# Performance work log

Hardware: AMD Instinct MI355X
Metric: run time of the kernel (lower is better)

The kernel has to match this reference:

```python
import jax, jax.numpy as jnp
import numpy as np

NMS_MAX_OUTPUTS = 2000
CLS_SCORE_THRESH = 0.7
IOU_THRESH = 0.3
USE_SIDE_REFINE = False
B, N_ANCHORS, N_VALID, NUM_CLASSES = 4, 20000, 12000, 2


def setup_inputs() -> dict:
    key = jax.random.key(0)
    k = jax.random.split(key, 7)
    deltas = 0.5 * jax.random.normal(k[0], (B, N_ANCHORS, 2), jnp.float32)
    side_deltas = 0.5 * jax.random.normal(k[1], (B, N_ANCHORS, 1), jnp.float32)
    class_logits = 2.0 * jax.random.normal(k[2], (B, N_ANCHORS, NUM_CLASSES), jnp.float32)
    # CTPN-style anchors: fixed width 16, heights in [11, 280], on a ~1600px page
    cx = jax.random.uniform(k[3], (N_VALID,), jnp.float32, 8.0, 1592.0)
    cy = jax.random.uniform(k[4], (N_VALID,), jnp.float32, 0.0, 1600.0)
    h = jax.random.uniform(k[5], (N_VALID,), jnp.float32, 11.0, 280.0)
    valid_anchors = jnp.stack([cx - 8.0, cy - h * 0.5, cx + 8.0, cy + h * 0.5], axis=1)
    valid_indices = jnp.sort(
        jax.random.choice(k[6], N_ANCHORS, (N_VALID,), replace=False)
    ).astype(jnp.int32)
    return {
        "deltas": deltas,
        "side_deltas": side_deltas,
        "class_logits": class_logits,
        "valid_anchors": valid_anchors,
        "valid_indices": valid_indices,
    }


def apply_regress(deltas, side_deltas, anchors, use_side_refine):
    # deltas [B,V,2], side_deltas [B,V,1], anchors [V,4] -> [B,V,4]
    w = anchors[:, 2] - anchors[:, 0]
    h = anchors[:, 3] - anchors[:, 1]
    cx = (anchors[:, 0] + anchors[:, 2]) * 0.5
    cy = (anchors[:, 1] + anchors[:, 3]) * 0.5
    d = jnp.concatenate([deltas, side_deltas], axis=-1) * jnp.array([0.1, 0.2, 0.1], deltas.dtype)
    dy, dh, dx = d[..., 0], d[..., 1], d[..., 2]
    cy = cy + dy * h
    cx = cx + dx * w
    h = h * jnp.exp(dh)
    y1 = cy - h * 0.5
    y2 = cy + h * 0.5
    if use_side_refine:
        x1 = jnp.maximum(cx - w * 0.5, 0.0)
        x2 = cx + w * 0.5
    else:
        x1 = jnp.broadcast_to(anchors[:, 0], y1.shape)
        x2 = jnp.broadcast_to(anchors[:, 2], y1.shape)
    return jnp.stack([x1, y1, x2, y2], axis=-1)


def nms_single(boxes, scores, logits, max_out, iou_t, score_t):
    """Greedy NMS (tf.image.non_max_suppression semantics) + gather + pad_to_fixed_size."""
    V = boxes.shape[0]
    order = jnp.argsort(-jax.lax.stop_gradient(scores))
    b, s, l = boxes[order], scores[order], logits[order]
    bc = jax.lax.stop_gradient(b)  # suppression decisions are non-differentiable
    x1, y1, x2, y2 = bc[:, 0], bc[:, 1], bc[:, 2], bc[:, 3]
    areas = (x2 - x1) * (y2 - y1)
    idxs = jnp.arange(V)
    valid = jax.lax.stop_gradient(s) > score_t

    def body(i, keep):
        xx1 = jnp.maximum(x1[i], x1)
        yy1 = jnp.maximum(y1[i], y1)
        xx2 = jnp.minimum(x2[i], x2)
        yy2 = jnp.minimum(y2[i], y2)
        inter = jnp.maximum(xx2 - xx1, 0.0) * jnp.maximum(yy2 - yy1, 0.0)
        iou = inter / (areas[i] + areas - inter + 1e-10)
        sup = (iou > iou_t) & (idxs > i)
        return jnp.where(keep[i], keep & ~sup, keep)

    keep = jax.lax.fori_loop(0, V, body, valid)
    rank = jnp.cumsum(keep.astype(jnp.int32)) - 1
    sel = keep & (rank < max_out)
    dest = jnp.where(sel, rank, max_out)  # overflow rows parked at row max_out, sliced off
    tag = jnp.ones((V, 1), b.dtype)

    def pad_fixed(x):
        # append tag column of 1s for real rows, scatter to fixed size, zero-pad rest
        aug = jnp.where(sel[:, None], jnp.concatenate([x, tag], axis=1), 0.0)
        out = jnp.zeros((max_out + 1, aug.shape[1]), aug.dtype).at[dest].set(aug)
        return out[:max_out]

    return pad_fixed(b), pad_fixed(s[:, None]), pad_fixed(l)


def reference(deltas, side_deltas, class_logits, valid_anchors, valid_indices):
    d = jnp.take(deltas, valid_indices, axis=1)
    sd = jnp.take(side_deltas, valid_indices, axis=1)
    cl = jnp.take(class_logits, valid_indices, axis=1)
    class_scores = jax.nn.softmax(cl, axis=-1)
    fg_scores = jnp.max(class_scores[..., 1:], axis=-1)  # [B,V]
    proposals = apply_regress(d, sd, valid_anchors, USE_SIDE_REFINE)  # [B,V,4]
    f = lambda bb, ss, ll: nms_single(bb, ss, ll, NMS_MAX_OUTPUTS, IOU_THRESH, CLS_SCORE_THRESH)
    boxes, box_scores, out_logits = jax.vmap(f)(proposals, fg_scores, cl)
    return boxes, box_scores, out_logits
```

## Files before the change

kernel.cpp:

```cpp
#include <hip/hip_runtime.h>
#include <cstdint>
#include <cstddef>

typedef unsigned long long u64;
typedef unsigned int u32;
typedef u32 u32x4 __attribute__((ext_vector_type(4)));

#define AS1 __attribute__((address_space(1)))
#define AS3 __attribute__((address_space(3)))

constexpr int kB = 4;
constexpr int kNA = 20000;
constexpr int kV = 12000;
constexpr int kCAP = 5120;
constexpr int kW = kCAP / 64;
constexpr int kIC = 256;
constexpr int kMAXOUT = 2000;
constexpr int kGPB = 20;
constexpr float kIOU = 0.3f;
constexpr float kSCORE = 0.7f;

static __device__ __forceinline__ u64 greedy64(u64 freeS, u32 d_lo, u32 d_hi) {
  u64 keptS;
  asm volatile(
      "s_mov_b64 s[40:41], %[free]\n\t"
      "s_mov_b64 s[42:43], 0\n\t"
      "GRD_%=:\n\t"
      "s_ff1_i32_b64 s44, s[40:41]\n\t"
      "s_cmp_eq_i32 s44, -1\n\t"
      "s_cbranch_scc1 GRDEND_%=\n\t"
      "s_bitset1_b64 s[42:43], s44\n\t"
      "s_bitset0_b64 s[40:41], s44\n\t"
      "v_readlane_b32 s46, %[dlo], s44\n\t"
      "v_readlane_b32 s47, %[dhi], s44\n\t"
      "s_nop 4\n\t"
      "s_andn2_b64 s[40:41], s[40:41], s[46:47]\n\t"
      "s_branch GRD_%=\n\t"
      "GRDEND_%=:\n\t"
      "s_mov_b64 %[kept], s[42:43]\n\t"
      : [kept] "=&s"(keptS)
      : [free] "s"(freeS), [dlo] "v"(d_lo), [dhi] "v"(d_hi)
      : "s40", "s41", "s42", "s43", "s44", "s45", "s46", "s47", "scc");
  return keptS;
}

__device__ __forceinline__ u64 waveOr64(u64 v) {
  v |= __shfl_xor((unsigned long long)v, 32, 64);
  v |= __shfl_xor((unsigned long long)v, 16, 64);
  v |= __shfl_xor((unsigned long long)v, 8, 64);
  v |= __shfl_xor((unsigned long long)v, 4, 64);
  v |= __shfl_xor((unsigned long long)v, 2, 64);
  v |= __shfl_xor((unsigned long long)v, 1, 64);
  return v;
}

__device__ __forceinline__ u64 readlane64u(u64 v, int l) {
  u32 lo = __builtin_amdgcn_readlane((u32)v, (u32)l);
  u32 hi = __builtin_amdgcn_readlane((u32)(v >> 32), (u32)l);
  return ((u64)hi << 32) | lo;
}

__global__ __launch_bounds__(256) void stage_score(
    const float* __restrict__ deltas, const float* __restrict__ logits,
    const float* __restrict__ anchors, const int* __restrict__ vidx,
    u32* __restrict__ counts, u64* __restrict__ keys,
    float* __restrict__ rec_y1, float* __restrict__ rec_y2,
    float* __restrict__ rec_l0, float* __restrict__ rec_l1) {
  int t = blockIdx.x * 256 + threadIdx.x;
  if (t >= kB * kV) return;
  int b = t / kV, i = t - b * kV;
  int lane = threadIdx.x & 63;
  int idx = vidx[i];
  float2 lg = *(const float2*)(logits + ((size_t)b * kNA + idx) * 2);
  float score = 1.0f / (1.0f + expf(lg.x - lg.y));
  if (!(score > kSCORE)) return;
  float2 dd = *(const float2*)(deltas + ((size_t)b * kNA + idx) * 2);
  float4 a = *(const float4*)(anchors + (size_t)i * 4);
  float h = a.w - a.y;
  float cy = (a.y + a.w) * 0.5f + (dd.x * 0.1f) * h;
  float hn = h * expf(dd.y * 0.2f);
  rec_y1[t] = cy - hn * 0.5f;
  rec_y2[t] = cy + hn * 0.5f;
  rec_l0[t] = lg.x;
  rec_l1[t] = lg.y;
  u64 act = __ballot(1);
  int b0 = (int)__builtin_amdgcn_readfirstlane((u32)b);
  u64 sameb = __ballot(b == b0);
  u64 grp = (b == b0) ? sameb : (act & ~sameb);
  u32 cnt = (u32)__popcll(grp);
  int lead = (int)__ffsll((unsigned long long)grp) - 1;
  u32 base = 0;
  if (lane == lead) base = atomicAdd(&counts[b], cnt);
  base = (u32)__shfl((int)base, lead, 64);
  u32 pos = base + (u32)__popcll(grp & ((1ULL << lane) - 1ULL));
  if (pos < kCAP) {
    u64 key = ((u64)(0xFFFFFFFFu - __float_as_uint(score)) << 32) | (u32)i;
    keys[(size_t)b * kCAP + pos] = key;
  }
}

__global__ __launch_bounds__(256) void rank_sort_emit(
    const u32* __restrict__ counts, const u64* __restrict__ keys,
    const float* __restrict__ rec_y1, const float* __restrict__ rec_y2,
    const float* __restrict__ rec_l0, const float* __restrict__ rec_l1,
    const float* __restrict__ anchors,
    float4* __restrict__ sbox, float* __restrict__ sarea,
    float* __restrict__ ssc, float* __restrict__ sl0, float* __restrict__ sl1) {
  __shared__ u64 sk[kCAP];
  int b = blockIdx.x / (kCAP / 256);
  int chunk = blockIdx.x % (kCAP / 256);
  int tid = threadIdx.x;
  int cnt = (int)min(counts[b], (u32)kCAP);
  for (int e = tid; e < kCAP; e += 256)
    sk[e] = (e < cnt) ? keys[(size_t)b * kCAP + e] : ~0ULL;
  __syncthreads();
  int s = chunk * 256 + tid;
  if (s >= cnt) return;
  u64 ks = sk[s];
  int rank = 0;
  for (int j = 0; j < kCAP; j += 8) {
#pragma unroll
    for (int u = 0; u < 8; ++u) rank += (sk[j + u] < ks) ? 1 : 0;
  }
  int i = (int)(u32)ks;
  float sc = __uint_as_float(0xFFFFFFFFu - (u32)(ks >> 32));
  float x1 = anchors[(size_t)i * 4 + 0], x2 = anchors[(size_t)i * 4 + 2];
  float y1 = rec_y1[b * kV + i], y2 = rec_y2[b * kV + i];
  size_t o = (size_t)b * kCAP + rank;
  sbox[o] = make_float4(x1, y1, x2, y2);
  sarea[o] = (x2 - x1) * (y2 - y1);
  ssc[o] = sc;
  sl0[o] = rec_l0[b * kV + i];
  sl1[o] = rec_l1[b * kV + i];
}

__global__ __launch_bounds__(256) void stage_mask(
    const u32* __restrict__ counts,
    const float4* __restrict__ sbox, const float* __restrict__ sarea,
    u64* __restrict__ mask) {
  __shared__ float4 sb[4][kIC];
  __shared__ float sa[4][kIC];
  int lane = threadIdx.x & 63;
  int wv = threadIdx.x >> 6;
  int gw = blockIdx.x * 4 + wv;
  int bt = gw & 3;
  int rest = gw >> 2;
  int jb = rest % kW;
  int ic = rest / kW;
  int M = (int)min(counts[bt], (u32)kCAP);
  int W = (M + 63) >> 6;
  if (jb >= W) return;
  int ibeg = ic * kIC;
  int iend = min(min(M, jb * 64 + 64), ibeg + kIC);
  if (ibeg >= iend) return;
  const float4* pb = sbox + (size_t)bt * kCAP;
  const float* pa = sarea + (size_t)bt * kCAP;
  u64* mb = mask + (size_t)bt * ((size_t)kW * kCAP);
#pragma unroll
  for (int r = 0; r < kIC / 64; ++r) {
    int e = r * 64 + lane;
    sb[wv][e] = pb[ibeg + e];
    sa[wv][e] = pa[ibeg + e];
  }
  int j = jb * 64 + lane;
  bool jv = (j < M);
  float4 bj = make_float4(0.f, 0.f, 0.f, 0.f);
  float aj = 0.f;
  if (jv) { bj = pb[j]; aj = pa[j]; }
  for (int b0 = ibeg; b0 < iend; b0 += 64) {
    int lim = min(iend - b0, 64);
    u64 mywm = 0;
#pragma unroll 4
    for (int k = 0; k < lim; ++k) {
      int e = b0 - ibeg + k;
      float4 bi = sb[wv][e];
      float ai = sa[wv][e];
      float xx1 = fmaxf(bi.x, bj.x);
      float yy1 = fmaxf(bi.y, bj.y);
      float xx2 = fminf(bi.z, bj.z);
      float yy2 = fminf(bi.w, bj.w);
      float inter = fmaxf(xx2 - xx1, 0.0f) * fmaxf(yy2 - yy1, 0.0f);
      float iou = inter / (ai + aj - inter + 1e-10f);
      bool sup = jv && (j > b0 + k) && (iou > kIOU);
      u64 wm = __ballot(sup);
      if (k == lane) mywm = wm;
    }
    if (lane < lim)
      mb[(((size_t)(b0 >> 6)) * kW + jb) * 64 + lane] = mywm;
  }
}

__global__ __launch_bounds__(64, 1) void stage_scan(
    const u32* __restrict__ counts, const u64* __restrict__ mask,
    u64* __restrict__ pub,
    const float4* __restrict__ sbox, const float* __restrict__ ssc,
    const float* __restrict__ sl0, const float* __restrict__ sl1,
    float* __restrict__ out) {
  __shared__ __align__(16) u64 col[20224];
  const int bid = blockIdx.x;
  const int bt = bid & 3;
  const int g = bid >> 2;
  const int lane = threadIdx.x;
  const int M = (int)min(counts[bt], (u32)kCAP);
  const int W = (M + 63) >> 6;
  const int blk0 = 4 * g;
  if (blk0 >= W) return;
  const u64* mb = mask + (size_t)bt * ((size_t)kW * kCAP);
  u64* pp = pub + (size_t)(bt * kGPB) * 8;

  const int nu = min(4 * g + 4, 78);
  for (int b = 0; b < nu; ++b) {
    __builtin_amdgcn_global_load_lds(
        (const AS1 u32*)(mb + ((size_t)b * kW + blk0) * 64 + (size_t)lane * 2),
        (AS3 u32*)&col[b * 256], 16, 0, 0);
    __builtin_amdgcn_global_load_lds(
        (const AS1 u32*)(mb + ((size_t)b * kW + blk0 + 2) * 64 + (size_t)lane * 2),
        (AS3 u32*)&col[b * 256 + 128], 16, 0, 0);
  }
  if (g == 19) {
    __builtin_amdgcn_global_load_lds(
        (const AS1 u32*)(mb + ((size_t)78 * kW + 78) * 64 + (size_t)lane * 2),
        (AS3 u32*)&col[19968], 16, 0, 0);
    __builtin_amdgcn_global_load_lds(
        (const AS1 u32*)(mb + ((size_t)79 * kW + 78) * 64 + (size_t)lane * 2),
        (AS3 u32*)&col[20096], 16, 0, 0);
  }
  __builtin_amdgcn_s_waitcnt(0x0070);

  auto wpv = [&](int b, int wq) -> const u64* {
    if (b >= 78) return &col[19968 + (b - 78) * 128 + (wq - 2) * 64];
    return &col[b * 256 + wq * 64];
  };

  u64 acc0 = 0, acc1 = 0, acc2 = 0, acc3 = 0;
  u32 cum = 0;
  const u64* qa = pp + (size_t)lane * 2;
  const u64* qb = pp + 128 + (size_t)(lane & 15) * 2;
  int next = 0;
  while (next < g) {
    u32x4 ra, rb;
    asm volatile(
        "global_load_dwordx4 %0, %2, off sc0 sc1\n\t"
        "global_load_dwordx4 %1, %3, off sc0 sc1\n\t"
        "s_waitcnt vmcnt(0)"
        : "=&v"(ra), "=&v"(rb)
        : "v"(qa), "v"(qb)
        : "memory");
    u64 wA0 = ((u64)ra[1] << 32) | ra[0];
    u64 wA1 = ((u64)ra[3] << 32) | ra[2];
    u64 wB0 = ((u64)rb[1] << 32) | rb[0];
    u64 wB1 = ((u64)rb[3] << 32) | rb[2];
    u64 okA = __ballot(((wA0 & wA1) >> 63) != 0);
    u64 okB = __ballot(((wB0 & wB1) >> 63) != 0);
    int w = next;
    for (; w < g; ++w) {
      u64 km0, km1, km2, km3;
      if (w < 16) {
        if (((okA >> (4 * w)) & 0xFULL) != 0xFULL) break;
        int L = 4 * w;
        km0 = (u64)(u32)readlane64u(wA0, L)     | ((u64)(u32)readlane64u(wA1, L) << 32);
        km1 = (u64)(u32)readlane64u(wA0, L + 1) | ((u64)(u32)readlane64u(wA1, L + 1) << 32);
        km2 = (u64)(u32)readlane64u(wA0, L + 2) | ((u64)(u32)readlane64u(wA1, L + 2) << 32);
        km3 = (u64)(u32)readlane64u(wA0, L + 3) | ((u64)(u32)readlane64u(wA1, L + 3) << 32);
      } else {
        int L = 4 * (w - 16);
        if (((okB >> L) & 0xFULL) != 0xFULL) break;
        km0 = (u64)(u32)readlane64u(wB0, L)     | ((u64)(u32)readlane64u(wB1, L) << 32);
        km1 = (u64)(u32)readlane64u(wB0, L + 1) | ((u64)(u32)readlane64u(wB1, L + 1) << 32);
        km2 = (u64)(u32)readlane64u(wB0, L + 2) | ((u64)(u32)readlane64u(wB1, L + 2) << 32);
        km3 = (u64)(u32)readlane64u(wB0, L + 3) | ((u64)(u32)readlane64u(wB1, L + 3) << 32);
      }
      cum += (u32)__popcll(km0) + (u32)__popcll(km1) +
             (u32)__popcll(km2) + (u32)__popcll(km3);
      if (km0 | km1 | km2 | km3) {
        u64 m0 = -(u64)((km0 >> lane) & 1ULL);
        u64 m1 = -(u64)((km1 >> lane) & 1ULL);
        u64 m2 = -(u64)((km2 >> lane) & 1ULL);
        u64 m3 = -(u64)((km3 >> lane) & 1ULL);
        const u64* p0 = &col[(4 * w + 0) * 256];
        const u64* p1 = &col[(4 * w + 1) * 256];
        const u64* p2 = &col[(4 * w + 2) * 256];
        const u64* p3 = &col[(4 * w + 3) * 256];
        u64 v0 = (p0[lane] & m0) | (p1[lane] & m1) | (p2[lane] & m2) | (p3[lane] & m3);
        u64 v1 = (p0[64 + lane] & m0) | (p1[64 + lane] & m1) | (p2[64 + lane] & m2) | (p3[64 + lane] & m3);
        u64 v2 = (p0[128 + lane] & m0) | (p1[128 + lane] & m1) | (p2[128 + lane] & m2) | (p3[128 + lane] & m3);
        u64 v3 = (p0[192 + lane] & m0) | (p1[192 + lane] & m1) | (p2[192 + lane] & m2) | (p3[192 + lane] & m3);
        acc0 |= waveOr64(v0);
        acc1 |= waveOr64(v1);
        acc2 |= waveOr64(v2);
        acc3 |= waveOr64(v3);
      }
    }
    next = w;
    if (next < g) __builtin_amdgcn_s_sleep(8);
  }

  u64 km[4];
  u32 cums[4];
#define OWN_BLOCK(J, ACC)                                                     \
  {                                                                           \
    const int blk = blk0 + (J);                                               \
    cums[J] = cum;                                                            \
    u64 k = 0;                                                                \
    if (blk < W && (int)cum < kMAXOUT) {                                      \
      int remn = M - blk * 64;                                                \
      u64 validm = (remn >= 64) ? ~0ULL : ((1ULL << remn) - 1ULL);            \
      u64 freeb = ~(ACC)&validm;                                              \
      u32 flo = __builtin_amdgcn_readfirstlane((u32)freeb);                   \
      u32 fhi = __builtin_amdgcn_readfirstlane((u32)(freeb >> 32));           \
      u64 diag = wpv(blk, J)[lane];                                           \
      k = greedy64(((u64)fhi << 32) | flo, (u32)diag, (u32)(diag >> 32));     \
    }                                                                         \
    km[J] = k;                                                                \
    cum += (u32)__popcll(k);                                                  \
  }
  OWN_BLOCK(0, acc0)
  if (km[0]) {
    u64 m = -(u64)((km[0] >> lane) & 1ULL);
    acc1 |= waveOr64(wpv(blk0, 1)[lane] & m);
    acc2 |= waveOr64(wpv(blk0, 2)[lane] & m);
    acc3 |= waveOr64(wpv(blk0, 3)[lane] & m);
  }
  OWN_BLOCK(1, acc1)
  if (km[1]) {
    u64 m = -(u64)((km[1] >> lane) & 1ULL);
    acc2 |= waveOr64(wpv(blk0 + 1, 2)[lane] & m);
    acc3 |= waveOr64(wpv(blk0 + 1, 3)[lane] & m);
  }
  OWN_BLOCK(2, acc2)
  if (km[2]) {
    u64 m = -(u64)((km[2] >> lane) & 1ULL);
    acc3 |= waveOr64(wpv(blk0 + 2, 3)[lane] & m);
  }
  OWN_BLOCK(3, acc3)
#undef OWN_BLOCK

  if (lane == 0) {
    const u64 F = 1ULL << 63;
#pragma unroll
    for (int c = 0; c < 4; ++c) {
      (void)__hip_atomic_fetch_or(&pp[(size_t)g * 8 + 2 * c], F | (u64)(u32)km[c],
                                  __ATOMIC_RELAXED, __HIP_MEMORY_SCOPE_AGENT);
      (void)__hip_atomic_fetch_or(&pp[(size_t)g * 8 + 2 * c + 1], F | (u64)(u32)(km[c] >> 32),
                                  __ATOMIC_RELAXED, __HIP_MEMORY_SCOPE_AGENT);
    }
  }

  float* boxes = out;
  float* bscores = out + (size_t)kB * kMAXOUT * 5;
  float* blogits = out + (size_t)kB * kMAXOUT * 7;
  auto emit = [&](int i, int rank) {
    size_t o = (size_t)bt * kCAP + i;
    float4 bx = sbox[o];
    size_t t = (size_t)bt * kMAXOUT + rank;
    boxes[t * 5 + 0] = bx.x;
    boxes[t * 5 + 1] = bx.y;
    boxes[t * 5 + 2] = bx.z;
    boxes[t * 5 + 3] = bx.w;
    boxes[t * 5 + 4] = 1.0f;
    bscores[t * 2 + 0] = ssc[o];
    bscores[t * 2 + 1] = 1.0f;
    blogits[t * 3 + 0] = sl0[o];
    blogits[t * 3 + 1] = sl1[o];
    blogits[t * 3 + 2] = 1.0f;
  };
#pragma unroll
  for (int c = 0; c < 4; ++c) {
    if ((km[c] >> lane) & 1ULL) {
      int rank = (int)cums[c] + (int)__popcll(km[c] & ((1ULL << lane) - 1ULL));
      if (rank < kMAXOUT) emit((blk0 + c) * 64 + lane, rank);
    }
  }
}

extern "C" void kernel_launch(void* const* d_in, const int* in_sizes, int n_in,
                              void* d_out, int out_size, void* d_ws, size_t ws_size,
                              hipStream_t stream) {
  const float* deltas = (const float*)d_in[0];
  const float* logits = (const float*)d_in[2];
  const float* anchors = (const float*)d_in[3];
  const int* vidx = (const int*)d_in[4];
  float* out = (float*)d_out;

  char* p = (char*)d_ws;
  auto take = [&](size_t bytes) -> char* {
    char* r = p;
    p += (bytes + 255) & ~(size_t)255;
    return r;
  };
  u32* counts = (u32*)take(kB * sizeof(u32));
  u64* pub = (u64*)take((size_t)kB * kGPB * 8 * sizeof(u64));
  u64* keys = (u64*)take((size_t)kB * kCAP * sizeof(u64));
  float* rec_y1 = (float*)take((size_t)kB * kV * sizeof(float));
  float* rec_y2 = (float*)take((size_t)kB * kV * sizeof(float));
  float* rec_l0 = (float*)take((size_t)kB * kV * sizeof(float));
  float* rec_l1 = (float*)take((size_t)kB * kV * sizeof(float));
  float4* sbox = (float4*)take((size_t)kB * kCAP * sizeof(float4));
  float* sarea = (float*)take((size_t)kB * kCAP * sizeof(float));
  float* ssc = (float*)take((size_t)kB * kCAP * sizeof(float));
  float* sl0 = (float*)take((size_t)kB * kCAP * sizeof(float));
  float* sl1 = (float*)take((size_t)kB * kCAP * sizeof(float));
  u64* mask = (u64*)take((size_t)kB * kCAP * kW * sizeof(u64) + 4096);

  (void)hipMemsetAsync(out, 0, (size_t)out_size * sizeof(float), stream);
  (void)hipMemsetAsync(counts, 0, 5376, stream);

  stage_score<<<(kB * kV + 255) / 256, 256, 0, stream>>>(
      deltas, logits, anchors, vidx, counts, keys, rec_y1, rec_y2, rec_l0, rec_l1);
  rank_sort_emit<<<kB * (kCAP / 256), 256, 0, stream>>>(
      counts, keys, rec_y1, rec_y2, rec_l0, rec_l1, anchors,
      sbox, sarea, ssc, sl0, sl1);
  stage_mask<<<kB * kW * (kCAP / kIC) / 4, 256, 0, stream>>>(
      counts, sbox, sarea, mask);
  stage_scan<<<kB * kGPB, 64, 0, stream>>>(
      counts, mask, pub, sbox, ssc, sl0, sl1, out);
}
```

Baseline: 339.2 us.

## Fuse IoU mask and greedy scan kernels with per-column completion counters

Merges the mask-building kernel and the scan kernel into one launch. Mask workgroups bump a per-column atomic counter when they finish, and scan workgroups (placed at the end of the grid) spin on those counters, so scanning of early columns can overlap with mask work on later columns. The scan side drops its bulk LDS prefetch of the mask and instead reads the needed mask words straight from global memory into registers. Risks include scan blocks spinning while holding CU slots, more global-load latency inside the serial scan loop, and possible deadlock if scan blocks are scheduled before the mask blocks they depend on.

```diff
diff --git a/kernel.cpp b/kernel.cpp
--- a/kernel.cpp
+++ b/kernel.cpp
@@ -15,8 +15,10 @@
 constexpr int kCAP = 5120;
 constexpr int kW = kCAP / 64;
 constexpr int kIC = 256;
+constexpr int kNCH = kCAP / kIC;
 constexpr int kMAXOUT = 2000;
 constexpr int kGPB = 20;
+constexpr int kMWG = kB * kW * kNCH / 4;
 constexpr float kIOU = 0.3f;
 constexpr float kSCORE = 0.7f;
 
@@ -134,72 +136,77 @@
   sl1[o] = rec_l1[b * kV + i];
 }
 
-__global__ __launch_bounds__(256) void stage_mask(
+__global__ __launch_bounds__(256) void fused_mask_scan(
     const u32* __restrict__ counts,
     const float4* __restrict__ sbox, const float* __restrict__ sarea,
-    u64* __restrict__ mask) {
-  __shared__ float4 sb[4][kIC];
-  __shared__ float sa[4][kIC];
-  int lane = threadIdx.x & 63;
-  int wv = threadIdx.x >> 6;
-  int gw = blockIdx.x * 4 + wv;
-  int bt = gw & 3;
-  int rest = gw >> 2;
-  int jb = rest % kW;
-  int ic = rest / kW;
-  int M = (int)min(counts[bt], (u32)kCAP);
-  int W = (M + 63) >> 6;
-  if (jb >= W) return;
-  int ibeg = ic * kIC;
-  int iend = min(min(M, jb * 64 + 64), ibeg + kIC);
-  if (ibeg >= iend) return;
-  const float4* pb = sbox + (size_t)bt * kCAP;
-  const float* pa = sarea + (size_t)bt * kCAP;
-  u64* mb = mask + (size_t)bt * ((size_t)kW * kCAP);
-#pragma unroll
-  for (int r = 0; r < kIC / 64; ++r) {
-    int e = r * 64 + lane;
-    sb[wv][e] = pb[ibeg + e];
-    sa[wv][e] = pa[ibeg + e];
-  }
-  int j = jb * 64 + lane;
-  bool jv = (j < M);
-  float4 bj = make_float4(0.f, 0.f, 0.f, 0.f);
-  float aj = 0.f;
-  if (jv) { bj = pb[j]; aj = pa[j]; }
-  for (int b0 = ibeg; b0 < iend; b0 += 64) {
-    int lim = min(iend - b0, 64);
-    u64 mywm = 0;
+    u64* __restrict__ mask, u32* __restrict__ colcnt, u64* __restrict__ pub,
+    const float* __restrict__ ssc, const float* __restrict__ sl0,
+    const float* __restrict__ sl1, float* __restrict__ out) {
+  __shared__ float4 sbc[4][kIC];
+  __shared__ float sac[4][kIC];
+  const int bid = blockIdx.x;
+
+  if (bid < kMWG) {
+    int lane = threadIdx.x & 63;
+    int wv = threadIdx.x >> 6;
+    int gw = bid * 4 + wv;
+    int bt = gw & 3;
+    int rest = gw >> 2;
+    int jb = rest % kW;
+    int ic = rest / kW;
+    int M = (int)min(counts[bt], (u32)kCAP);
+    int W = (M + 63) >> 6;
+    if (jb < W) {
+      int ibeg = ic * kIC;
+      int iend = min(min(M, jb * 64 + 64), ibeg + kIC);
+      if (ibeg < iend) {
+        const float4* pb = sbox + (size_t)bt * kCAP;
+        const float* pa = sarea + (size_t)bt * kCAP;
+        u64* mb = mask + (size_t)bt * ((size_t)kW * kCAP);
+#pragma unroll
+        for (int r = 0; r < kIC / 64; ++r) {
+          int e = r * 64 + lane;
+          sbc[wv][e] = pb[ibeg + e];
+          sac[wv][e] = pa[ibeg + e];
+        }
+        int j = jb * 64 + lane;
+        bool jv = (j < M);
+        float4 bj = make_float4(0.f, 0.f, 0.f, 0.f);
+        float aj = 0.f;
+        if (jv) { bj = pb[j]; aj = pa[j]; }
+        for (int b0 = ibeg; b0 < iend; b0 += 64) {
+          int lim = min(iend - b0, 64);
+          u64 mywm = 0;
 #pragma unroll 4
-    for (int k = 0; k < lim; ++k) {
-      int e = b0 - ibeg + k;
-      float4 bi = sb[wv][e];
-      float ai = sa[wv][e];
-      float xx1 = fmaxf(bi.x, bj.x);
-      float yy1 = fmaxf(bi.y, bj.y);
-      float xx2 = fminf(bi.z, bj.z);
-      float yy2 = fminf(bi.w, bj.w);
-      float inter = fmaxf(xx2 - xx1, 0.0f) * fmaxf(yy2 - yy1, 0.0f);
-      float iou = inter / (ai + aj - inter + 1e-10f);
-      bool sup = jv && (j > b0 + k) && (iou > kIOU);
-      u64 wm = __ballot(sup);
-      if (k == lane) mywm = wm;
+          for (int k = 0; k < lim; ++k) {
+            int e = b0 - ibeg + k;
+            float4 bi = sbc[wv][e];
+            float ai = sac[wv][e];
+            float xx1 = fmaxf(bi.x, bj.x);
+            float yy1 = fmaxf(bi.y, bj.y);
+            float xx2 = fminf(bi.z, bj.z);
+            float yy2 = fminf(bi.w, bj.w);
+            float inter = fmaxf(xx2 - xx1, 0.0f) * fmaxf(yy2 - yy1, 0.0f);
+            float iou = inter / (ai + aj - inter + 1e-10f);
+            bool sup = jv && (j > b0 + k) && (iou > kIOU);
+            u64 wm = __ballot(sup);
+            if (k == lane) mywm = wm;
+          }
+          if (lane < lim)
+            mb[(((size_t)(b0 >> 6)) * kW + jb) * 64 + lane] = mywm;
+        }
+      }
     }
-    if (lane < lim)
-      mb[(((size_t)(b0 >> 6)) * kW + jb) * 64 + lane] = mywm;
-  }
-}
-
-__global__ __launch_bounds__(64, 1) void stage_scan(
-    const u32* __restrict__ counts, const u64* __restrict__ mask,
-    u64* __restrict__ pub,
-    const float4* __restrict__ sbox, const float* __restrict__ ssc,
-    const float* __restrict__ sl0, const float* __restrict__ sl1,
-    float* __restrict__ out) {
-  __shared__ __align__(16) u64 col[20224];
-  const int bid = blockIdx.x;
-  const int bt = bid & 3;
-  const int g = bid >> 2;
+    if (lane == 0)
+      (void)__hip_atomic_fetch_add(&colcnt[bt * kW + jb], 1u, __ATOMIC_RELEASE,
+                                   __HIP_MEMORY_SCOPE_AGENT);
+    return;
+  }
+
+  if (threadIdx.x >= 64) return;
+  const int sid = bid - kMWG;
+  const int bt = sid & 3;
+  const int g = sid >> 2;
   const int lane = threadIdx.x;
   const int M = (int)min(counts[bt], (u32)kCAP);
   const int W = (M + 63) >> 6;
@@ -208,29 +215,20 @@
   const u64* mb = mask + (size_t)bt * ((size_t)kW * kCAP);
   u64* pp = pub + (size_t)(bt * kGPB) * 8;
 
-  const int nu = min(4 * g + 4, 78);
-  for (int b = 0; b < nu; ++b) {
-    __builtin_amdgcn_global_load_lds(
-        (const AS1 u32*)(mb + ((size_t)b * kW + blk0) * 64 + (size_t)lane * 2),
-        (AS3 u32*)&col[b * 256], 16, 0, 0);
-    __builtin_amdgcn_global_load_lds(
-        (const AS1 u32*)(mb + ((size_t)b * kW + blk0 + 2) * 64 + (size_t)lane * 2),
-        (AS3 u32*)&col[b * 256 + 128], 16, 0, 0);
-  }
-  if (g == 19) {
-    __builtin_amdgcn_global_load_lds(
-        (const AS1 u32*)(mb + ((size_t)78 * kW + 78) * 64 + (size_t)lane * 2),
-        (AS3 u32*)&col[19968], 16, 0, 0);
-    __builtin_amdgcn_global_load_lds(
-        (const AS1 u32*)(mb + ((size_t)79 * kW + 78) * 64 + (size_t)lane * 2),
-        (AS3 u32*)&col[20096], 16, 0, 0);
-  }
-  __builtin_amdgcn_s_waitcnt(0x0070);
-
-  auto wpv = [&](int b, int wq) -> const u64* {
-    if (b >= 78) return &col[19968 + (b - 78) * 128 + (wq - 2) * 64];
-    return &col[b * 256 + wq * 64];
-  };
+#pragma unroll
+  for (int c = 0; c < 4; ++c) {
+    const u32* cp = &colcnt[bt * kW + 4 * g + c];
+    while (__hip_atomic_load(cp, __ATOMIC_ACQUIRE, __HIP_MEMORY_SCOPE_AGENT) <
+           (u32)kNCH)
+      __builtin_amdgcn_s_sleep(16);
+  }
+
+  u64 own[4][4];
+#pragma unroll
+  for (int J = 0; J < 4; ++J)
+#pragma unroll
+    for (int q = 0; q < 4; ++q)
+      own[J][q] = mb[((size_t)(blk0 + J) * kW + 4 * g + q) * 64 + lane];
 
   u64 acc0 = 0, acc1 = 0, acc2 = 0, acc3 = 0;
   u32 cum = 0;
@@ -273,22 +271,20 @@
       cum += (u32)__popcll(km0) + (u32)__popcll(km1) +
              (u32)__popcll(km2) + (u32)__popcll(km3);
       if (km0 | km1 | km2 | km3) {
+        u64 v[4][4];
+#pragma unroll
+        for (int c = 0; c < 4; ++c)
+#pragma unroll
+          for (int q = 0; q < 4; ++q)
+            v[c][q] = mb[((size_t)(4 * w + c) * kW + 4 * g + q) * 64 + lane];
         u64 m0 = -(u64)((km0 >> lane) & 1ULL);
         u64 m1 = -(u64)((km1 >> lane) & 1ULL);
         u64 m2 = -(u64)((km2 >> lane) & 1ULL);
         u64 m3 = -(u64)((km3 >> lane) & 1ULL);
-        const u64* p0 = &col[(4 * w + 0) * 256];
-        const u64* p1 = &col[(4 * w + 1) * 256];
-        const u64* p2 = &col[(4 * w + 2) * 256];
-        const u64* p3 = &col[(4 * w + 3) * 256];
-        u64 v0 = (p0[lane] & m0) | (p1[lane] & m1) | (p2[lane] & m2) | (p3[lane] & m3);
-        u64 v1 = (p0[64 + lane] & m0) | (p1[64 + lane] & m1) | (p2[64 + lane] & m2) | (p3[64 + lane] & m3);
-        u64 v2 = (p0[128 + lane] & m0) | (p1[128 + lane] & m1) | (p2[128 + lane] & m2) | (p3[128 + lane] & m3);
-        u64 v3 = (p0[192 + lane] & m0) | (p1[192 + lane] & m1) | (p2[192 + lane] & m2) | (p3[192 + lane] & m3);
-        acc0 |= waveOr64(v0);
-        acc1 |= waveOr64(v1);
-        acc2 |= waveOr64(v2);
-        acc3 |= waveOr64(v3);
+        acc0 |= waveOr64((v[0][0] & m0) | (v[1][0] & m1) | (v[2][0] & m2) | (v[3][0] & m3));
+        acc1 |= waveOr64((v[0][1] & m0) | (v[1][1] & m1) | (v[2][1] & m2) | (v[3][1] & m3));
+        acc2 |= waveOr64((v[0][2] & m0) | (v[1][2] & m1) | (v[2][2] & m2) | (v[3][2] & m3));
+        acc3 |= waveOr64((v[0][3] & m0) | (v[1][3] & m1) | (v[2][3] & m2) | (v[3][3] & m3));
       }
     }
     next = w;
@@ -308,7 +304,7 @@
       u64 freeb = ~(ACC)&validm;                                              \
       u32 flo = __builtin_amdgcn_readfirstlane((u32)freeb);                   \
       u32 fhi = __builtin_amdgcn_readfirstlane((u32)(freeb >> 32));           \
-      u64 diag = wpv(blk, J)[lane];                                           \
+      u64 diag = own[J][J];                                                   \
       k = greedy64(((u64)fhi << 32) | flo, (u32)diag, (u32)(diag >> 32));     \
     }                                                                         \
     km[J] = k;                                                                \
@@ -317,20 +313,20 @@
   OWN_BLOCK(0, acc0)
   if (km[0]) {
     u64 m = -(u64)((km[0] >> lane) & 1ULL);
-    acc1 |= waveOr64(wpv(blk0, 1)[lane] & m);
-    acc2 |= waveOr64(wpv(blk0, 2)[lane] & m);
-    acc3 |= waveOr64(wpv(blk0, 3)[lane] & m);
+    acc1 |= waveOr64(own[0][1] & m);
+    acc2 |= waveOr64(own[0][2] & m);
+    acc3 |= waveOr64(own[0][3] & m);
   }
   OWN_BLOCK(1, acc1)
   if (km[1]) {
     u64 m = -(u64)((km[1] >> lane) & 1ULL);
-    acc2 |= waveOr64(wpv(blk0 + 1, 2)[lane] & m);
-    acc3 |= waveOr64(wpv(blk0 + 1, 3)[lane] & m);
+    acc2 |= waveOr64(own[1][2] & m);
+    acc3 |= waveOr64(own[1][3] & m);
   }
   OWN_BLOCK(2, acc2)
   if (km[2]) {
     u64 m = -(u64)((km[2] >> lane) & 1ULL);
-    acc3 |= waveOr64(wpv(blk0 + 2, 3)[lane] & m);
+    acc3 |= waveOr64(own[2][3] & m);
   }
   OWN_BLOCK(3, acc3)
 #undef OWN_BLOCK
@@ -341,7 +337,8 @@
     for (int c = 0; c < 4; ++c) {
       (void)__hip_atomic_fetch_or(&pp[(size_t)g * 8 + 2 * c], F | (u64)(u32)km[c],
                                   __ATOMIC_RELAXED, __HIP_MEMORY_SCOPE_AGENT);
-      (void)__hip_atomic_fetch_or(&pp[(size_t)g * 8 + 2 * c + 1], F | (u64)(u32)(km[c] >> 32),
+      (void)__hip_atomic_fetch_or(&pp[(size_t)g * 8 + 2 * c + 1],
+                                  F | (u64)(u32)(km[c] >> 32),
                                   __ATOMIC_RELAXED, __HIP_MEMORY_SCOPE_AGENT);
     }
   }
@@ -390,6 +387,7 @@
   };
   u32* counts = (u32*)take(kB * sizeof(u32));
   u64* pub = (u64*)take((size_t)kB * kGPB * 8 * sizeof(u64));
+  u32* colcnt = (u32*)take((size_t)kB * kW * sizeof(u32));
   u64* keys = (u64*)take((size_t)kB * kCAP * sizeof(u64));
   float* rec_y1 = (float*)take((size_t)kB * kV * sizeof(float));
   float* rec_y2 = (float*)take((size_t)kB * kV * sizeof(float));
@@ -403,15 +401,13 @@
   u64* mask = (u64*)take((size_t)kB * kCAP * kW * sizeof(u64) + 4096);
 
   (void)hipMemsetAsync(out, 0, (size_t)out_size * sizeof(float), stream);
-  (void)hipMemsetAsync(counts, 0, 5376, stream);
+  (void)hipMemsetAsync(counts, 0, 6656, stream);
 
   stage_score<<<(kB * kV + 255) / 256, 256, 0, stream>>>(
       deltas, logits, anchors, vidx, counts, keys, rec_y1, rec_y2, rec_l0, rec_l1);
   rank_sort_emit<<<kB * (kCAP / 256), 256, 0, stream>>>(
       counts, keys, rec_y1, rec_y2, rec_l0, rec_l1, anchors,
       sbox, sarea, ssc, sl0, sl1);
-  stage_mask<<<kB * kW * (kCAP / kIC) / 4, 256, 0, stream>>>(
-      counts, sbox, sarea, mask);
-  stage_scan<<<kB * kGPB, 64, 0, stream>>>(
-      counts, mask, pub, sbox, ssc, sl0, sl1, out);
-}
+  fused_mask_scan<<<kMWG + kB * kGPB, 256, 0, stream>>>(
+      counts, sbox, sarea, mask, colcnt, pub, ssc, sl0, sl1, out);
+}
```

Measured after the change: 347.0 us. 2.3% more time.

## Fuse score and rank kernels via atomic completion counter; zero output rows in scan

Applied to the files above, without the earlier changes.

Merges the scoring and rank-sort kernels into one launch. The rank workgroups spin on a global counter that the scoring workgroups increment with release semantics. It also removes the full-output memset and instead has the scan kernel zero the unused output rows, so one memset and one kernel launch go away. The spin-wait depends on all scoring workgroups being scheduled before the rank workgroups, which could deadlock or stall if dispatch order or residency does not allow that.

```diff
diff --git a/kernel.cpp b/kernel.cpp
--- a/kernel.cpp
+++ b/kernel.cpp
@@ -17,6 +17,8 @@
 constexpr int kIC = 256;
 constexpr int kMAXOUT = 2000;
 constexpr int kGPB = 20;
+constexpr int kSCWG = (kB * kV + 255) / 256;
+constexpr int kRWG = kB * (kCAP / 256);
 constexpr float kIOU = 0.3f;
 constexpr float kSCORE = 0.7f;
 
@@ -60,56 +62,75 @@
   return ((u64)hi << 32) | lo;
 }
 
-__global__ __launch_bounds__(256) void stage_score(
+__global__ __launch_bounds__(256) void score_rank(
     const float* __restrict__ deltas, const float* __restrict__ logits,
     const float* __restrict__ anchors, const int* __restrict__ vidx,
-    u32* __restrict__ counts, u64* __restrict__ keys,
+    u32* __restrict__ counts, u32* __restrict__ scoredone,
+    u64* __restrict__ keys,
     float* __restrict__ rec_y1, float* __restrict__ rec_y2,
-    float* __restrict__ rec_l0, float* __restrict__ rec_l1) {
-  int t = blockIdx.x * 256 + threadIdx.x;
-  if (t >= kB * kV) return;
-  int b = t / kV, i = t - b * kV;
-  int lane = threadIdx.x & 63;
-  int idx = vidx[i];
-  float2 lg = *(const float2*)(logits + ((size_t)b * kNA + idx) * 2);
-  float score = 1.0f / (1.0f + expf(lg.x - lg.y));
-  if (!(score > kSCORE)) return;
-  float2 dd = *(const float2*)(deltas + ((size_t)b * kNA + idx) * 2);
-  float4 a = *(const float4*)(anchors + (size_t)i * 4);
-  float h = a.w - a.y;
-  float cy = (a.y + a.w) * 0.5f + (dd.x * 0.1f) * h;
-  float hn = h * expf(dd.y * 0.2f);
-  rec_y1[t] = cy - hn * 0.5f;
-  rec_y2[t] = cy + hn * 0.5f;
-  rec_l0[t] = lg.x;
-  rec_l1[t] = lg.y;
-  u64 act = __ballot(1);
-  int b0 = (int)__builtin_amdgcn_readfirstlane((u32)b);
-  u64 sameb = __ballot(b == b0);
-  u64 grp = (b == b0) ? sameb : (act & ~sameb);
-  u32 cnt = (u32)__popcll(grp);
-  int lead = (int)__ffsll((unsigned long long)grp) - 1;
-  u32 base = 0;
-  if (lane == lead) base = atomicAdd(&counts[b], cnt);
-  base = (u32)__shfl((int)base, lead, 64);
-  u32 pos = base + (u32)__popcll(grp & ((1ULL << lane) - 1ULL));
-  if (pos < kCAP) {
-    u64 key = ((u64)(0xFFFFFFFFu - __float_as_uint(score)) << 32) | (u32)i;
-    keys[(size_t)b * kCAP + pos] = key;
-  }
-}
-
-__global__ __launch_bounds__(256) void rank_sort_emit(
-    const u32* __restrict__ counts, const u64* __restrict__ keys,
-    const float* __restrict__ rec_y1, const float* __restrict__ rec_y2,
-    const float* __restrict__ rec_l0, const float* __restrict__ rec_l1,
-    const float* __restrict__ anchors,
+    float* __restrict__ rec_l0, float* __restrict__ rec_l1,
     float4* __restrict__ sbox, float* __restrict__ sarea,
     float* __restrict__ ssc, float* __restrict__ sl0, float* __restrict__ sl1) {
   __shared__ u64 sk[kCAP];
-  int b = blockIdx.x / (kCAP / 256);
-  int chunk = blockIdx.x % (kCAP / 256);
-  int tid = threadIdx.x;
+  const int bid = blockIdx.x;
+  const int tid = threadIdx.x;
+
+  if (bid < kSCWG) {
+    int t = bid * 256 + tid;
+    int lane = tid & 63;
+    bool valid = t < kB * kV;
+    int b = 0, i = 0, idx = 0;
+    float score = 0.f;
+    float2 lg = make_float2(0.f, 0.f);
+    if (valid) {
+      b = t / kV;
+      i = t - b * kV;
+      idx = vidx[i];
+      lg = *(const float2*)(logits + ((size_t)b * kNA + idx) * 2);
+      score = 1.0f / (1.0f + expf(lg.x - lg.y));
+    }
+    bool pass = valid && (score > kSCORE);
+    if (pass) {
+      float2 dd = *(const float2*)(deltas + ((size_t)b * kNA + idx) * 2);
+      float4 a = *(const float4*)(anchors + (size_t)i * 4);
+      float h = a.w - a.y;
+      float cy = (a.y + a.w) * 0.5f + (dd.x * 0.1f) * h;
+      float hn = h * expf(dd.y * 0.2f);
+      rec_y1[t] = cy - hn * 0.5f;
+      rec_y2[t] = cy + hn * 0.5f;
+      rec_l0[t] = lg.x;
+      rec_l1[t] = lg.y;
+      u64 act = __ballot(1);
+      int b0 = (int)__builtin_amdgcn_readfirstlane((u32)b);
+      u64 sameb = __ballot(b == b0);
+      u64 grp = (b == b0) ? sameb : (act & ~sameb);
+      u32 cnt = (u32)__popcll(grp);
+      int lead = (int)__ffsll((unsigned long long)grp) - 1;
+      u32 base = 0;
+      if (lane == lead) base = atomicAdd(&counts[b], cnt);
+      base = (u32)__shfl((int)base, lead, 64);
+      u32 pos = base + (u32)__popcll(grp & ((1ULL << lane) - 1ULL));
+      if (pos < kCAP) {
+        u64 key = ((u64)(0xFFFFFFFFu - __float_as_uint(score)) << 32) | (u32)i;
+        keys[(size_t)b * kCAP + pos] = key;
+      }
+    }
+    __syncthreads();
+    if (tid == 0)
+      (void)__hip_atomic_fetch_add(scoredone, 1u, __ATOMIC_RELEASE,
+                                   __HIP_MEMORY_SCOPE_AGENT);
+    return;
+  }
+
+  if (tid == 0) {
+    while (__hip_atomic_load(scoredone, __ATOMIC_ACQUIRE,
+                             __HIP_MEMORY_SCOPE_AGENT) < (u32)kSCWG)
+      __builtin_amdgcn_s_sleep(32);
+  }
+  __syncthreads();
+  const int rbid = bid - kSCWG;
+  int b = rbid / (kCAP / 256);
+  int chunk = rbid % (kCAP / 256);
   int cnt = (int)min(counts[b], (u32)kCAP);
   for (int e = tid; e < kCAP; e += 256)
     sk[e] = (e < cnt) ? keys[(size_t)b * kCAP + e] : ~0ULL;
@@ -204,7 +225,21 @@
   const int M = (int)min(counts[bt], (u32)kCAP);
   const int W = (M + 63) >> 6;
   const int blk0 = 4 * g;
-  if (blk0 >= W) return;
+  float* boxes = out;
+  float* bscores = out + (size_t)kB * kMAXOUT * 5;
+  float* blogits = out + (size_t)kB * kMAXOUT * 7;
+  auto zrow = [&](int r) {
+    size_t t = (size_t)bt * kMAXOUT + r;
+    boxes[t * 5 + 0] = 0.f; boxes[t * 5 + 1] = 0.f; boxes[t * 5 + 2] = 0.f;
+    boxes[t * 5 + 3] = 0.f; boxes[t * 5 + 4] = 0.f;
+    bscores[t * 2 + 0] = 0.f; bscores[t * 2 + 1] = 0.f;
+    blogits[t * 3 + 0] = 0.f; blogits[t * 3 + 1] = 0.f; blogits[t * 3 + 2] = 0.f;
+  };
+  if (blk0 >= W) {
+    if (g == 0)
+      for (int r = lane; r < kMAXOUT; r += 64) zrow(r);
+    return;
+  }
   const u64* mb = mask + (size_t)bt * ((size_t)kW * kCAP);
   u64* pp = pub + (size_t)(bt * kGPB) * 8;
 
@@ -346,9 +381,6 @@
     }
   }
 
-  float* boxes = out;
-  float* bscores = out + (size_t)kB * kMAXOUT * 5;
-  float* blogits = out + (size_t)kB * kMAXOUT * 7;
   auto emit = [&](int i, int rank) {
     size_t o = (size_t)bt * kCAP + i;
     float4 bx = sbox[o];
@@ -371,6 +403,11 @@
       if (rank < kMAXOUT) emit((blk0 + c) * 64 + lane, rank);
     }
   }
+
+  if (g == ((W - 1) >> 2)) {
+    int kc = min((int)cum, kMAXOUT);
+    for (int r = kc + lane; r < kMAXOUT; r += 64) zrow(r);
+  }
 }
 
 extern "C" void kernel_launch(void* const* d_in, const int* in_sizes, int n_in,
@@ -390,6 +427,7 @@
   };
   u32* counts = (u32*)take(kB * sizeof(u32));
   u64* pub = (u64*)take((size_t)kB * kGPB * 8 * sizeof(u64));
+  u32* scoredone = (u32*)take(sizeof(u32));
   u64* keys = (u64*)take((size_t)kB * kCAP * sizeof(u64));
   float* rec_y1 = (float*)take((size_t)kB * kV * sizeof(float));
   float* rec_y2 = (float*)take((size_t)kB * kV * sizeof(float));
@@ -402,14 +440,11 @@
   float* sl1 = (float*)take((size_t)kB * kCAP * sizeof(float));
   u64* mask = (u64*)take((size_t)kB * kCAP * kW * sizeof(u64) + 4096);
 
-  (void)hipMemsetAsync(out, 0, (size_t)out_size * sizeof(float), stream);
-  (void)hipMemsetAsync(counts, 0, 5376, stream);
-
-  stage_score<<<(kB * kV + 255) / 256, 256, 0, stream>>>(
-      deltas, logits, anchors, vidx, counts, keys, rec_y1, rec_y2, rec_l0, rec_l1);
-  rank_sort_emit<<<kB * (kCAP / 256), 256, 0, stream>>>(
-      counts, keys, rec_y1, rec_y2, rec_l0, rec_l1, anchors,
-      sbox, sarea, ssc, sl0, sl1);
+  (void)hipMemsetAsync(counts, 0, 5632, stream);
+
+  score_rank<<<kSCWG + kRWG, 256, 0, stream>>>(
+      deltas, logits, anchors, vidx, counts, scoredone, keys,
+      rec_y1, rec_y2, rec_l0, rec_l1, sbox, sarea, ssc, sl0, sl1);
   stage_mask<<<kB * kW * (kCAP / kIC) / 4, 256, 0, stream>>>(
       counts, sbox, sarea, mask);
   stage_scan<<<kB * kGPB, 64, 0, stream>>>(
```

Result: no change. 345.4 us (+1.8%).
